# Optimization experiments

Hardware: AMD Instinct MI355X
Metric: run time of the kernel (lower is better)

Reference implementation:

```python
import jax, jax.numpy as jnp
from jax import lax
import numpy as np

N_LAYERS = 64
T_END = 1.0
NF = 512
NF2 = NF // 2
BATCH = 8192
H = T_END / N_LAYERS  # step size h


def setup_inputs() -> dict:
    key = jax.random.key(0)
    k1, k2, k3 = jax.random.split(key, 3)
    Y0 = jax.random.normal(k1, (BATCH, NF), dtype=jnp.float32)
    K = jax.random.normal(k2, (NF2, NF2, N_LAYERS), dtype=jnp.float32)
    b = jax.random.normal(k3, (NF, 1, N_LAYERS), dtype=jnp.float32)
    return {"Y0": Y0, "K": K, "b": b}


def reference(Y0, K, b):
    # Y0: [B, nf]; split into Y (first half) and Z (second half).
    Y = Y0[:, :NF2]
    Z = Y0[:, NF2:]
    Ks = jnp.moveaxis(K, -1, 0)          # [L, nf2, nf2]
    bs = jnp.moveaxis(b[:, 0, :], -1, 0)  # [L, nf]

    def step(carry, kb):
        Yc, Zc = carry
        Kj, bj = kb
        # Z <- Z + h * tanh(Y @ Kj^T + b_lower)   (F.linear(Y, Kj, b[nf2:]))
        Zn = Zc + H * jnp.tanh(Yc @ Kj.T + bj[NF2:])
        # Y <- Y + h * tanh(-(Z @ Kj) + b_upper)  (F.linear(Z, -Kj^T, b[:nf2]))
        Yn = Yc + H * jnp.tanh(-(Zn @ Kj) + bj[:NF2])
        return (Yn, Zn), None

    (Y, Z), _ = lax.scan(step, (Y, Z), (Ks, bs))
    return jnp.concatenate([Y, Z], axis=1)
```

## Files before the change

### kernel.cpp

```cpp
#include <hip/hip_runtime.h>


typedef _Float16 f16x8 __attribute__((ext_vector_type(8)));
typedef _Float16 f16x2 __attribute__((ext_vector_type(2)));
typedef float    f32x4 __attribute__((ext_vector_type(4)));

#define H_STEP 0.015625f

#define ST_Y   0
#define ST_Z   8192
#define BUF0   16384
#define BIASO  49152

__device__ __forceinline__ float fast_tanh(float x) {
    float xc = fminf(fmaxf(x, -9.0f), 9.0f);
    float t  = __builtin_amdgcn_exp2f(xc * 2.8853900817779268f);
    return (t - 1.0f) * __builtin_amdgcn_rcpf(t + 1.0f);
}

__device__ __forceinline__ int swz(int m, int k) {
    return (m << 8) + (k ^ ((m & 7) << 3));
}

__device__ __forceinline__ void gload16(const _Float16* g, _Float16* l) {
    __builtin_amdgcn_global_load_lds(
        (const __attribute__((address_space(1))) unsigned int*)g,
        (__attribute__((address_space(3))) unsigned int*)l, 16, 0, 0);
}
__device__ __forceinline__ void gload4(const float* g, _Float16* l) {
    __builtin_amdgcn_global_load_lds(
        (const __attribute__((address_space(1))) unsigned int*)g,
        (__attribute__((address_space(3))) unsigned int*)l, 4, 0, 0);
}

__global__ __launch_bounds__(256) void prep_split(
    const float* __restrict__ K,
    _Float16* __restrict__ B1h, _Float16* __restrict__ B2h)
{
    __shared__ float tile[32][33][9];
    const int a0 = (blockIdx.x & 7) << 5;
    const int b0 = ((blockIdx.x >> 3) & 7) << 5;
    const int j0 = (blockIdx.x >> 6) << 3;
    const int t = threadIdx.x;

    for (int idx = t; idx < 8192; idx += 256) {
        const int jj = idx & 7, bb = (idx >> 3) & 31, aa = idx >> 8;
        tile[aa][bb][jj] = K[((size_t)(a0 + aa) * 256 + (b0 + bb)) * 64 + (j0 + jj)];
    }
    __syncthreads();

    {
        const int w1 = a0 >> 5, kt = b0 >> 5;
        for (int idx = t; idx < 4096; idx += 256) {
            const int p = idx & 15, aa = (idx >> 4) & 31, jj = idx >> 9;
            const int kl = 2 * p, c = kl >> 3, e = kl & 7;
            const int u = aa * 4 + (c ^ ((aa >> 1) & 3));
            const size_t off = ((size_t)((j0 + jj) * 8 + kt)) * 8192 + w1 * 1024 + u * 8 + e;
            const f16x2 hv = {(_Float16)tile[aa][kl][jj], (_Float16)tile[aa][kl + 1][jj]};
            *(f16x2*)(B1h + off) = hv;
        }
    }
    {
        const int w2 = b0 >> 5, kt = a0 >> 5;
        for (int idx = t; idx < 4096; idx += 256) {
            const int p = idx & 15, bb = (idx >> 4) & 31, jj = idx >> 9;
            const int kl = 2 * p, c = kl >> 3, e = kl & 7;
            const int u = bb * 4 + (c ^ ((bb >> 1) & 3));
            const size_t off = ((size_t)((j0 + jj) * 8 + kt)) * 8192 + w2 * 1024 + u * 8 + e;
            const f16x2 hv = {(_Float16)tile[kl][bb][jj], (_Float16)tile[kl + 1][bb][jj]};
            *(f16x2*)(B2h + off) = hv;
        }
    }
}

#define MFMA16(A, B, C) __builtin_amdgcn_mfma_f32_16x16x32_f16((A), (B), (C), 0, 0, 0)
#define SBAR __builtin_amdgcn_sched_barrier(0)
#define WAITV(N) { asm volatile("s_waitcnt vmcnt(" #N ")" ::: "memory"); SBAR; }
#define WAITL(N) { asm volatile("s_waitcnt lgkmcnt(" #N ")" ::: "memory"); SBAR; }

#define LOADF(A0, A1, B0, B1, PK)                                               \
    {                                                                           \
        const int k0_ = (PK) * 32 + hi4 * 8;                                    \
        const _Float16* bb_ = lds + BUF0 + ((PK) & 3) * 8192 + bfw;             \
        B0 = *(const f16x8*)(bb_ + bf0);                                        \
        B1 = *(const f16x8*)(bb_ + bf1);                                        \
        A0 = *(const f16x8*)(lds + stA + swz(l15, k0_));                        \
        A1 = *(const f16x8*)(lds + stA + swz(16 + l15, k0_));                   \
    }

#define DMAT(T)                                                                 \
    {                                                                           \
        const _Float16* sb_ = ((T) < 8) ? Bc : Bn;                              \
        _Float16* db_ = lds + BUF0 + ((T) & 3) * 8192 + gdst;                   \
        gload16(sb_ + ((T) & 7) * 8192 + gsrc,       db_);                      \
        gload16(sb_ + ((T) & 7) * 8192 + gsrc + 512, db_ + 512);                \
    }

#define FMAS(A0, A1, B0, B1)                                                    \
    accH00 = MFMA16(A0, B0, accH00);                                            \
    accH01 = MFMA16(A0, B1, accH01);                                            \
    accH10 = MFMA16(A1, B0, accH10);                                            \
    accH11 = MFMA16(A1, B1, accH11);

template<bool NEG>
__device__ __forceinline__ void phase(
    _Float16* lds, const int stA, const int stO,
    const _Float16* __restrict__ Bc,
    const _Float16* __restrict__ Bn,
    const float* __restrict__ biasG,
    float (&M)[2][2][4],
    const int w, const int l15, const int hi4,
    const int bfw, const int bf0, const int bf1,
    const int gsrc, const int gdst, const size_t bsrc)
{
    f32x4 accH00 = {0.f,0.f,0.f,0.f}, accH01 = {0.f,0.f,0.f,0.f};
    f32x4 accH10 = {0.f,0.f,0.f,0.f}, accH11 = {0.f,0.f,0.f,0.f};

    f16x8 a00,a01,b00,b01;
    f16x8 a10,a11,b10,b11;
    f16x8 a20,a21,b20,b21;

    WAITV(4)
    LOADF(a00,a01,b00,b01, 0)
    LOADF(a10,a11,b10,b11, 1)

    WAITV(2) WAITL(4)
    gload4(biasG + bsrc, lds + BIASO + (w << 7));
    DMAT(4)  LOADF(a20,a21,b20,b21, 2)  FMAS(a00,a01,b00,b01)
    WAITV(3) WAITL(4)
    DMAT(5)  LOADF(a00,a01,b00,b01, 3)  FMAS(a10,a11,b10,b11)
    WAITV(2) WAITL(4)
    DMAT(6)  LOADF(a10,a11,b10,b11, 4)  FMAS(a20,a21,b20,b21)
    WAITV(2) WAITL(4)
    DMAT(7)  LOADF(a20,a21,b20,b21, 5)  FMAS(a00,a01,b00,b01)
    WAITV(2) WAITL(4)
    DMAT(8)  LOADF(a00,a01,b00,b01, 6)  FMAS(a10,a11,b10,b11)
    WAITV(2) WAITL(4)
    DMAT(9)  LOADF(a10,a11,b10,b11, 7)  FMAS(a20,a21,b20,b21)
    WAITL(4)
    DMAT(10) FMAS(a00,a01,b00,b01)
    WAITL(0)
    DMAT(11) FMAS(a10,a11,b10,b11)

    const float* bp = (const float*)(lds + BIASO + (w << 7));
    const float bv0 = bp[l15], bv1 = bp[l15 + 16];

#pragma unroll
    for (int mt = 0; mt < 2; ++mt) {
#pragma unroll
        for (int nt = 0; nt < 2; ++nt) {
            const f32x4 s4 = (mt == 0) ? ((nt == 0) ? accH00 : accH01)
                                       : ((nt == 0) ? accH10 : accH11);
            const float bv = nt ? bv1 : bv0;
            const int n = (w << 5) + nt * 16 + l15;
#pragma unroll
            for (int q = 0; q < 4; ++q) {
                const float x = NEG ? (bv - s4[q]) : (s4[q] + bv);
                const float v = M[mt][nt][q] + H_STEP * fast_tanh(x);
                M[mt][nt][q] = v;
                const int m = mt * 16 + hi4 * 4 + q;
                lds[stO + swz(m, n)] = (_Float16)v;
            }
        }
    }
    asm volatile("s_waitcnt lgkmcnt(0)" ::: "memory");
    __builtin_amdgcn_s_barrier();
    SBAR;
}

__global__ __launch_bounds__(512, 2) void ms1_main(
    const float* __restrict__ Y0,
    const float* __restrict__ bvec,
    const _Float16* __restrict__ B1h, const _Float16* __restrict__ B2h,
    float* __restrict__ out)
{
    extern __shared__ _Float16 lds[];

    const int tid  = threadIdx.x;
    const int lane = tid & 63, w = tid >> 6;
    const int l15 = lane & 15, hi4 = lane >> 4;
    const size_t row0 = (size_t)blockIdx.x * 32;

    const int bfw = w << 10;
    const int c0 = l15, c1 = 16 + l15;
    const int bf0 = (c0 * 4 + (hi4 ^ ((c0 >> 1) & 3))) * 8;
    const int bf1 = (c1 * 4 + (hi4 ^ ((c1 >> 1) & 3))) * 8;
    const int gsrc = (w << 10) + lane * 8;
    const int gdst = (w << 10);
    const size_t bsrc = (size_t)((w << 5) + (lane & 31)) * 64;

    float Ym[2][2][4], Zm[2][2][4];

#pragma unroll
    for (int mt = 0; mt < 2; ++mt) {
#pragma unroll
        for (int nt = 0; nt < 2; ++nt) {
            const int n = (w << 5) + nt * 16 + l15;
#pragma unroll
            for (int q = 0; q < 4; ++q) {
                const int m = mt * 16 + hi4 * 4 + q;
                const size_t base = (row0 + m) * 512;
                const float y = Y0[base + n];
                const float z = Y0[base + 256 + n];
                Ym[mt][nt][q] = y; Zm[mt][nt][q] = z;
                lds[ST_Y + swz(m, n)] = (_Float16)y;
            }
        }
    }
    __syncthreads();

#pragma unroll
    for (int t0 = 0; t0 < 4; ++t0) {
        _Float16* db = lds + BUF0 + t0 * 8192 + gdst;
        gload16(B1h + t0 * 8192 + gsrc,       db);
        gload16(B1h + t0 * 8192 + gsrc + 512, db + 512);
    }

    for (int j = 0; j < 64; ++j) {
        const _Float16* C1 = B1h + (size_t)j * 65536;
        const _Float16* C2 = B2h + (size_t)j * 65536;
        const int jn = (j < 63) ? j + 1 : 0;
        phase<false>(lds, ST_Y, ST_Z, C1, C2, bvec + 256 * 64 + j, Zm,
                     w, l15, hi4, bfw, bf0, bf1, gsrc, gdst, bsrc);
        phase<true>(lds, ST_Z, ST_Y, C2, B1h + (size_t)jn * 65536,
                    bvec + j, Ym,
                    w, l15, hi4, bfw, bf0, bf1, gsrc, gdst, bsrc);
    }

#pragma unroll
    for (int mt = 0; mt < 2; ++mt) {
#pragma unroll
        for (int nt = 0; nt < 2; ++nt) {
            const int n = (w << 5) + nt * 16 + l15;
#pragma unroll
            for (int q = 0; q < 4; ++q) {
                const int m = mt * 16 + hi4 * 4 + q;
                const size_t base = (row0 + m) * 512;
                out[base + n]       = Ym[mt][nt][q];
                out[base + 256 + n] = Zm[mt][nt][q];
            }
        }
    }
}

extern "C" void kernel_launch(void* const* d_in, const int* in_sizes, int n_in,
                              void* d_out, int out_size, void* d_ws, size_t ws_size,
                              hipStream_t stream) {
    (void)in_sizes; (void)n_in; (void)out_size;
    const float* Y0 = (const float*)d_in[0];
    const float* K  = (const float*)d_in[1];
    const float* b  = (const float*)d_in[2];

    const size_t ARR = (size_t)64 * 256 * 256;
    if (ws_size < 2 * ARR * sizeof(_Float16)) return;

    _Float16* B1h = (_Float16*)d_ws;
    _Float16* B2h = B1h + ARR;

    hipFuncSetAttribute((const void*)ms1_main,
                        hipFuncAttributeMaxDynamicSharedMemorySize, 100352);

    prep_split<<<512, 256, 0, stream>>>(K, B1h, B2h);
    ms1_main<<<256, 512, 100352, stream>>>(Y0, b, B1h, B2h, (float*)d_out);
}
```

Measured before the change: 283.5 us.

## Load weight fragments directly into registers instead of staging through LDS

Replaces the global-to-LDS DMA staging of the fp16 weight tiles with per-lane global_load_dwordx4 straight into registers. The loads are double-buffered across k-steps, and the next phase's first two tiles are prefetched across the phase boundary. This drops the LDS ring buffer, shrinking shared memory from about 100KB to about 34KB, and removes LDS reads for B. In exchange it relies on global/L2 latency being hidden by only two k-steps of lookahead, and each wave issues its own uncoalesced-pattern vector loads.

```diff
diff --git a/kernel.cpp b/kernel.cpp
--- a/kernel.cpp
+++ b/kernel.cpp
@@ -9,8 +9,7 @@
 
 #define ST_Y   0
 #define ST_Z   8192
-#define BUF0   16384
-#define BIASO  49152
+#define BIASO  16384
 
 __device__ __forceinline__ float fast_tanh(float x) {
     float xc = fminf(fmaxf(x, -9.0f), 9.0f);
@@ -22,15 +21,17 @@
     return (m << 8) + (k ^ ((m & 7) << 3));
 }
 
-__device__ __forceinline__ void gload16(const _Float16* g, _Float16* l) {
-    __builtin_amdgcn_global_load_lds(
-        (const __attribute__((address_space(1))) unsigned int*)g,
-        (__attribute__((address_space(3))) unsigned int*)l, 16, 0, 0);
-}
 __device__ __forceinline__ void gload4(const float* g, _Float16* l) {
     __builtin_amdgcn_global_load_lds(
         (const __attribute__((address_space(1))) unsigned int*)g,
         (__attribute__((address_space(3))) unsigned int*)l, 4, 0, 0);
+}
+
+__device__ __forceinline__ f16x8 gload_async(const _Float16* p) {
+    f16x8 r;
+    asm volatile("global_load_dwordx4 %0, %1, off"
+                 : "=v"(r) : "v"(p) : "memory");
+    return r;
 }
 
 __global__ __launch_bounds__(256) void prep_split(
@@ -78,22 +79,11 @@
 #define WAITV(N) { asm volatile("s_waitcnt vmcnt(" #N ")" ::: "memory"); SBAR; }
 #define WAITL(N) { asm volatile("s_waitcnt lgkmcnt(" #N ")" ::: "memory"); SBAR; }
 
-#define LOADF(A0, A1, B0, B1, PK)                                               \
+#define LOADA(A0, A1, PK)                                                       \
     {                                                                           \
         const int k0_ = (PK) * 32 + hi4 * 8;                                    \
-        const _Float16* bb_ = lds + BUF0 + ((PK) & 3) * 8192 + bfw;             \
-        B0 = *(const f16x8*)(bb_ + bf0);                                        \
-        B1 = *(const f16x8*)(bb_ + bf1);                                        \
         A0 = *(const f16x8*)(lds + stA + swz(l15, k0_));                        \
         A1 = *(const f16x8*)(lds + stA + swz(16 + l15, k0_));                   \
-    }
-
-#define DMAT(T)                                                                 \
-    {                                                                           \
-        const _Float16* sb_ = ((T) < 8) ? Bc : Bn;                              \
-        _Float16* db_ = lds + BUF0 + ((T) & 3) * 8192 + gdst;                   \
-        gload16(sb_ + ((T) & 7) * 8192 + gsrc,       db_);                      \
-        gload16(sb_ + ((T) & 7) * 8192 + gsrc + 512, db_ + 512);                \
     }
 
 #define FMAS(A0, A1, B0, B1)                                                    \
@@ -101,6 +91,10 @@
     accH01 = MFMA16(A0, B1, accH01);                                            \
     accH10 = MFMA16(A1, B0, accH10);                                            \
     accH11 = MFMA16(A1, B1, accH11);
+
+#define BLOAD(BA, BB, SRC, T)                                                   \
+    BA = gload_async((SRC) + (T) * 8192 + pb0);                                 \
+    BB = gload_async((SRC) + (T) * 8192 + pb1);
 
 template<bool NEG>
 __device__ __forceinline__ void phase(
@@ -109,38 +103,56 @@
     const _Float16* __restrict__ Bn,
     const float* __restrict__ biasG,
     float (&M)[2][2][4],
+    f16x8& b0a, f16x8& b0b, f16x8& b1a, f16x8& b1b,
     const int w, const int l15, const int hi4,
-    const int bfw, const int bf0, const int bf1,
-    const int gsrc, const int gdst, const size_t bsrc)
+    const int pb0, const int pb1, const size_t bsrc)
 {
     f32x4 accH00 = {0.f,0.f,0.f,0.f}, accH01 = {0.f,0.f,0.f,0.f};
     f32x4 accH10 = {0.f,0.f,0.f,0.f}, accH11 = {0.f,0.f,0.f,0.f};
 
-    f16x8 a00,a01,b00,b01;
-    f16x8 a10,a11,b10,b11;
-    f16x8 a20,a21,b20,b21;
-
-    WAITV(4)
-    LOADF(a00,a01,b00,b01, 0)
-    LOADF(a10,a11,b10,b11, 1)
-
-    WAITV(2) WAITL(4)
+    f16x8 ca0, ca1, na0, na1;
+    LOADA(ca0, ca1, 0)
+
+    WAITV(2)
+    LOADA(na0, na1, 1)
+    WAITL(2)
+    FMAS(ca0, ca1, b0a, b0b)
+    BLOAD(b0a, b0b, Bc, 2) SBAR;
     gload4(biasG + bsrc, lds + BIASO + (w << 7));
-    DMAT(4)  LOADF(a20,a21,b20,b21, 2)  FMAS(a00,a01,b00,b01)
-    WAITV(3) WAITL(4)
-    DMAT(5)  LOADF(a00,a01,b00,b01, 3)  FMAS(a10,a11,b10,b11)
-    WAITV(2) WAITL(4)
-    DMAT(6)  LOADF(a10,a11,b10,b11, 4)  FMAS(a20,a21,b20,b21)
-    WAITV(2) WAITL(4)
-    DMAT(7)  LOADF(a20,a21,b20,b21, 5)  FMAS(a00,a01,b00,b01)
-    WAITV(2) WAITL(4)
-    DMAT(8)  LOADF(a00,a01,b00,b01, 6)  FMAS(a10,a11,b10,b11)
-    WAITV(2) WAITL(4)
-    DMAT(9)  LOADF(a10,a11,b10,b11, 7)  FMAS(a20,a21,b20,b21)
-    WAITL(4)
-    DMAT(10) FMAS(a00,a01,b00,b01)
+    WAITV(3)
+    LOADA(ca0, ca1, 2)
+    WAITL(2)
+    FMAS(na0, na1, b1a, b1b)
+    BLOAD(b1a, b1b, Bc, 3)
+    WAITV(3)
+    LOADA(na0, na1, 3)
+    WAITL(2)
+    FMAS(ca0, ca1, b0a, b0b)
+    BLOAD(b0a, b0b, Bc, 4)
+    WAITV(2)
+    LOADA(ca0, ca1, 4)
+    WAITL(2)
+    FMAS(na0, na1, b1a, b1b)
+    BLOAD(b1a, b1b, Bc, 5)
+    WAITV(2)
+    LOADA(na0, na1, 5)
+    WAITL(2)
+    FMAS(ca0, ca1, b0a, b0b)
+    BLOAD(b0a, b0b, Bc, 6)
+    WAITV(2)
+    LOADA(ca0, ca1, 6)
+    WAITL(2)
+    FMAS(na0, na1, b1a, b1b)
+    BLOAD(b1a, b1b, Bc, 7)
+    WAITV(2)
+    LOADA(na0, na1, 7)
+    WAITL(2)
+    FMAS(ca0, ca1, b0a, b0b)
+    BLOAD(b0a, b0b, Bn, 0)
+    WAITV(2)
     WAITL(0)
-    DMAT(11) FMAS(a10,a11,b10,b11)
+    FMAS(na0, na1, b1a, b1b)
+    BLOAD(b1a, b1b, Bn, 1)
 
     const float* bp = (const float*)(lds + BIASO + (w << 7));
     const float bv0 = bp[l15], bv1 = bp[l15 + 16];
@@ -174,19 +186,16 @@
     const _Float16* __restrict__ B1h, const _Float16* __restrict__ B2h,
     float* __restrict__ out)
 {
-    extern __shared__ _Float16 lds[];
+    __shared__ _Float16 lds[17408];
 
     const int tid  = threadIdx.x;
     const int lane = tid & 63, w = tid >> 6;
     const int l15 = lane & 15, hi4 = lane >> 4;
     const size_t row0 = (size_t)blockIdx.x * 32;
 
-    const int bfw = w << 10;
     const int c0 = l15, c1 = 16 + l15;
-    const int bf0 = (c0 * 4 + (hi4 ^ ((c0 >> 1) & 3))) * 8;
-    const int bf1 = (c1 * 4 + (hi4 ^ ((c1 >> 1) & 3))) * 8;
-    const int gsrc = (w << 10) + lane * 8;
-    const int gdst = (w << 10);
+    const int pb0 = (w << 10) + (c0 * 4 + (hi4 ^ ((c0 >> 1) & 3))) * 8;
+    const int pb1 = (w << 10) + (c1 * 4 + (hi4 ^ ((c1 >> 1) & 3))) * 8;
     const size_t bsrc = (size_t)((w << 5) + (lane & 31)) * 64;
 
     float Ym[2][2][4], Zm[2][2][4];
@@ -209,22 +218,19 @@
     }
     __syncthreads();
 
-#pragma unroll
-    for (int t0 = 0; t0 < 4; ++t0) {
-        _Float16* db = lds + BUF0 + t0 * 8192 + gdst;
-        gload16(B1h + t0 * 8192 + gsrc,       db);
-        gload16(B1h + t0 * 8192 + gsrc + 512, db + 512);
-    }
+    f16x8 b0a, b0b, b1a, b1b;
+    BLOAD(b0a, b0b, B1h, 0)
+    BLOAD(b1a, b1b, B1h, 1)
 
     for (int j = 0; j < 64; ++j) {
         const _Float16* C1 = B1h + (size_t)j * 65536;
         const _Float16* C2 = B2h + (size_t)j * 65536;
         const int jn = (j < 63) ? j + 1 : 0;
         phase<false>(lds, ST_Y, ST_Z, C1, C2, bvec + 256 * 64 + j, Zm,
-                     w, l15, hi4, bfw, bf0, bf1, gsrc, gdst, bsrc);
+                     b0a, b0b, b1a, b1b, w, l15, hi4, pb0, pb1, bsrc);
         phase<true>(lds, ST_Z, ST_Y, C2, B1h + (size_t)jn * 65536,
                     bvec + j, Ym,
-                    w, l15, hi4, bfw, bf0, bf1, gsrc, gdst, bsrc);
+                    b0a, b0b, b1a, b1b, w, l15, hi4, pb0, pb1, bsrc);
     }
 
 #pragma unroll
@@ -257,9 +263,6 @@
     _Float16* B1h = (_Float16*)d_ws;
     _Float16* B2h = B1h + ARR;
 
-    hipFuncSetAttribute((const void*)ms1_main,
-                        hipFuncAttributeMaxDynamicSharedMemorySize, 100352);
-
     prep_split<<<512, 256, 0, stream>>>(K, B1h, B2h);
-    ms1_main<<<256, 512, 100352, stream>>>(Y0, b, B1h, B2h, (float*)d_out);
-}
+    ms1_main<<<256, 512, 0, stream>>>(Y0, b, B1h, B2h, (float*)d_out);
+}
```

Measured after the change: 311.7 us. 9.9% more time.
